# Kernel tuning notes

Measured on AMD Instinct MI355X. Metric: run time of the kernel, lower is better.

## Reference

```python
import jax, jax.numpy as jnp
import numpy as np

B, T, D = 4, 4096, 64

def setup_inputs() -> dict:
    key = jax.random.key(0)
    kq, kk, kv = jax.random.split(key, 3)
    Q = jax.random.normal(kq, (B, T, D), dtype=jnp.float32)
    K = jax.random.normal(kk, (B, T, D), dtype=jnp.float32)
    V = jax.random.normal(kv, (B, T, D), dtype=jnp.float32)
    mask = jnp.zeros((B, T, T), dtype=jnp.float32)
    return {"Q": Q, "K": K, "V": V, "mask": mask}

def reference(Q, K, V, mask):
    dk = Q.shape[-1]
    # NOTE: original scales by 1/dk (not 1/sqrt(dk)) -- reproduce faithfully.
    scores = jnp.einsum('btd,bsd->bts', Q, K) * (1.0 / dk)  # [B,T,T]
    scores = scores + mask
    attn = jax.nn.softmax(scores, axis=-1)
    return jnp.einsum('bts,bsd->btd', attn, V)  # [B,T,D]
```

## Files before the change

kernel.cpp:

```cpp
#include <hip/hip_runtime.h>
#include <stdint.h>

#define BB 4
#define TT 4096
#define DD 64
#define KBLK 64

typedef short short8 __attribute__((ext_vector_type(8)));
typedef float f32x4 __attribute__((ext_vector_type(4)));

__device__ __forceinline__ uint16_t f2bf(float x) {
  uint32_t u = __float_as_uint(x);
  u += 0x7FFFu + ((u >> 16) & 1u);
  return (uint16_t)(u >> 16);
}
__device__ __forceinline__ float bf2f(uint16_t h) {
  return __uint_as_float(((uint32_t)h) << 16);
}

#define MFMA(a, b, c) __builtin_amdgcn_mfma_f32_16x16x32_bf16((a), (b), (c), 0, 0, 0)

__global__ __launch_bounds__(256) void prep_kernel(
    const float* __restrict__ Q, const float* __restrict__ K, const float* __restrict__ V,
    uint16_t* __restrict__ Qh, uint16_t* __restrict__ Ql,
    uint16_t* __restrict__ Kh, uint16_t* __restrict__ Kl,
    uint16_t* __restrict__ Vh, uint16_t* __restrict__ Vl) {
  __shared__ float vt[64][65];
  const int blk = blockIdx.x;
  const int b = blk >> 6;
  const int r0 = (blk & 63) << 6;
  const int t = threadIdx.x;
  const size_t base = ((size_t)b * TT + r0) * DD;
  for (int i = t; i < 64 * 64; i += 256) {
    float q = Q[base + i] * 0.015625f;
    uint16_t h = f2bf(q);
    Qh[base + i] = h;
    Ql[base + i] = f2bf(q - bf2f(h));
    float k = K[base + i];
    h = f2bf(k);
    Kh[base + i] = h;
    Kl[base + i] = f2bf(k - bf2f(h));
    int r = i >> 6, c = i & 63;
    vt[r][c] = V[base + i];
  }
  __syncthreads();
  for (int i = t; i < 64 * 64; i += 256) {
    int d = i >> 6, c = i & 63;
    float v = vt[c][d];
    uint16_t h = f2bf(v);
    size_t o = ((size_t)b * DD + d) * TT + r0 + c;
    Vh[o] = h;
    Vl[o] = f2bf(v - bf2f(h));
  }
}

template <int NSEG, int NW>
__global__ __launch_bounds__(NW * 64, 4) void attn_kernel(
    const float* __restrict__ mask, float* __restrict__ out,
    float* __restrict__ Op, float* __restrict__ Mp, float* __restrict__ Lp,
    const uint16_t* __restrict__ Qh, const uint16_t* __restrict__ Ql,
    const uint16_t* __restrict__ Kh, const uint16_t* __restrict__ Kl,
    const uint16_t* __restrict__ Vh, const uint16_t* __restrict__ Vl) {
  constexpr int RPB = NW * 16;
  constexpr int PBH = (TT / RPB) / 2;
  constexpr int SEGLEN = TT / NSEG;
  constexpr int NIT = SEGLEN / KBLK;

  __shared__ uint16_t Kh_s[64][72], Kl_s[64][72];
  __shared__ uint16_t Vh_s[64][72], Vl_s[64][72];
  __shared__ uint16_t Ph_s[NW][16][72], Pl_s[NW][16][72];

  const int bid = blockIdx.x;
  const int xcd = bid & 7;
  const int b = xcd >> 1;
  const int u = bid >> 3;
  const int rbl = (u % PBH) * 2 + (xcd & 1);
  const int seg = u / PBH;
  const int q0 = rbl * RPB;
  const int t = threadIdx.x;
  const int w = t >> 6;
  const int l = t & 63;
  const int lr = l & 15;
  const int lq = l >> 4;
  const int qrow = q0 + w * 16;
  const int sb = seg * SEGLEN;

  const uint16_t* qhp = Qh + ((size_t)b * TT + qrow + lr) * DD + lq * 8;
  const uint16_t* qlp = Ql + ((size_t)b * TT + qrow + lr) * DD + lq * 8;
  short8 qh[2], ql[2];
  qh[0] = *(const short8*)(qhp);
  qh[1] = *(const short8*)(qhp + 32);
  ql[0] = *(const short8*)(qlp);
  ql[1] = *(const short8*)(qlp + 32);

  f32x4 o[4];
  float mrow[4], lrow[4];
#pragma unroll
  for (int dt = 0; dt < 4; ++dt) o[dt] = (f32x4){0.f, 0.f, 0.f, 0.f};
#pragma unroll
  for (int j = 0; j < 4; ++j) { mrow[j] = -1e30f; lrow[j] = 0.f; }

  const float* mp[4];
#pragma unroll
  for (int j = 0; j < 4; ++j)
    mp[j] = mask + ((size_t)b * TT + qrow + lq * 4 + j) * TT + sb + lr;

  float mk[16];
#pragma unroll
  for (int tt = 0; tt < 4; ++tt)
#pragma unroll
    for (int j = 0; j < 4; ++j)
      mk[tt * 4 + j] = __builtin_nontemporal_load(mp[j] + tt * 16);

  const size_t kvb = (size_t)b * TT * DD;
  const size_t vtb = (size_t)b * DD * TT;

  for (int it = 0; it < NIT; ++it) {
    const int s0 = sb + it * KBLK;
    __syncthreads();
    for (int i = t; i < 512; i += NW * 64) {
      const int row = i >> 3, c = i & 7;
      const size_t ko = kvb + (size_t)(s0 + row) * DD + c * 8;
      *(short8*)&Kh_s[row][c * 8] = *(const short8*)(Kh + ko);
      *(short8*)&Kl_s[row][c * 8] = *(const short8*)(Kl + ko);
      const size_t vo = vtb + (size_t)row * TT + s0 + c * 8;
      *(short8*)&Vh_s[row][c * 8] = *(const short8*)(Vh + vo);
      *(short8*)&Vl_s[row][c * 8] = *(const short8*)(Vl + vo);
    }
    __syncthreads();

    float mk2[16];
    if (it + 1 < NIT) {
#pragma unroll
      for (int tt = 0; tt < 4; ++tt)
#pragma unroll
        for (int j = 0; j < 4; ++j)
          mk2[tt * 4 + j] = __builtin_nontemporal_load(mp[j] + (it + 1) * KBLK + tt * 16);
    } else {
#pragma unroll
      for (int i = 0; i < 16; ++i) mk2[i] = 0.f;
    }

    f32x4 s[4];
#pragma unroll
    for (int tt = 0; tt < 4; ++tt) {
      f32x4 acc = (f32x4){0.f, 0.f, 0.f, 0.f};
#pragma unroll
      for (int c = 0; c < 2; ++c) {
        const short8 bh = *(const short8*)&Kh_s[tt * 16 + lr][c * 32 + lq * 8];
        const short8 bl = *(const short8*)&Kl_s[tt * 16 + lr][c * 32 + lq * 8];
        acc = MFMA(qh[c], bh, acc);
        acc = MFMA(ql[c], bh, acc);
        acc = MFMA(qh[c], bl, acc);
      }
      s[tt] = acc;
    }
#pragma unroll
    for (int tt = 0; tt < 4; ++tt)
#pragma unroll
      for (int j = 0; j < 4; ++j) s[tt][j] += mk[tt * 4 + j];

    float cm[4];
#pragma unroll
    for (int j = 0; j < 4; ++j)
      cm[j] = fmaxf(fmaxf(s[0][j], s[1][j]), fmaxf(s[2][j], s[3][j]));
#pragma unroll
    for (int d = 1; d < 16; d <<= 1)
#pragma unroll
      for (int j = 0; j < 4; ++j) cm[j] = fmaxf(cm[j], __shfl_xor(cm[j], d, 16));
    float scl[4];
#pragma unroll
    for (int j = 0; j < 4; ++j) {
      const float mn = fmaxf(mrow[j], cm[j]);
      scl[j] = __expf(mrow[j] - mn);
      mrow[j] = mn;
    }
#pragma unroll
    for (int tt = 0; tt < 4; ++tt)
#pragma unroll
      for (int j = 0; j < 4; ++j) s[tt][j] = __expf(s[tt][j] - mrow[j]);
    float rs[4];
#pragma unroll
    for (int j = 0; j < 4; ++j) rs[j] = (s[0][j] + s[1][j]) + (s[2][j] + s[3][j]);
#pragma unroll
    for (int d = 1; d < 16; d <<= 1)
#pragma unroll
      for (int j = 0; j < 4; ++j) rs[j] += __shfl_xor(rs[j], d, 16);
#pragma unroll
    for (int j = 0; j < 4; ++j) lrow[j] = lrow[j] * scl[j] + rs[j];
#pragma unroll
    for (int dt = 0; dt < 4; ++dt)
#pragma unroll
      for (int j = 0; j < 4; ++j) o[dt][j] *= scl[j];

#pragma unroll
    for (int tt = 0; tt < 4; ++tt)
#pragma unroll
      for (int j = 0; j < 4; ++j) {
        const float p = s[tt][j];
        const uint16_t h = f2bf(p);
        Ph_s[w][lq * 4 + j][tt * 16 + lr] = h;
        Pl_s[w][lq * 4 + j][tt * 16 + lr] = f2bf(p - bf2f(h));
      }

#pragma unroll
    for (int c = 0; c < 2; ++c) {
      const short8 ph = *(const short8*)&Ph_s[w][lr][c * 32 + lq * 8];
      const short8 pl = *(const short8*)&Pl_s[w][lr][c * 32 + lq * 8];
#pragma unroll
      for (int dt = 0; dt < 4; ++dt) {
        const short8 vh = *(const short8*)&Vh_s[dt * 16 + lr][c * 32 + lq * 8];
        const short8 vl = *(const short8*)&Vl_s[dt * 16 + lr][c * 32 + lq * 8];
        o[dt] = MFMA(ph, vh, o[dt]);
        o[dt] = MFMA(pl, vh, o[dt]);
        o[dt] = MFMA(ph, vl, o[dt]);
      }
    }

#pragma unroll
    for (int i = 0; i < 16; ++i) mk[i] = mk2[i];
  }

  if constexpr (NSEG == 1) {
#pragma unroll
    for (int j = 0; j < 4; ++j) {
      const float inv = 1.0f / lrow[j];
      const size_t ob = ((size_t)b * TT + qrow + lq * 4 + j) * DD + lr;
#pragma unroll
      for (int dt = 0; dt < 4; ++dt) out[ob + dt * 16] = o[dt][j] * inv;
    }
  } else {
    const int grow = b * TT + qrow + lq * 4;
#pragma unroll
    for (int j = 0; j < 4; ++j) {
      const size_t r = (size_t)seg * (BB * TT) + grow + j;
#pragma unroll
      for (int dt = 0; dt < 4; ++dt) Op[r * 64 + dt * 16 + lr] = o[dt][j];
      if (lr == 0) { Mp[r] = mrow[j]; Lp[r] = lrow[j]; }
    }
  }
}

__global__ __launch_bounds__(256) void combine_kernel(
    const float* __restrict__ Op, const float* __restrict__ Mp,
    const float* __restrict__ Lp, float* __restrict__ out, int nseg) {
  const int gid = blockIdx.x * 256 + threadIdx.x;
  const int r = gid >> 6, d = gid & 63;
  constexpr int ROWS = BB * TT;
  float m = -3.0e38f;
  for (int s = 0; s < nseg; ++s) m = fmaxf(m, Mp[s * ROWS + r]);
  float num = 0.f, den = 0.f;
  for (int s = 0; s < nseg; ++s) {
    const float e = __expf(Mp[s * ROWS + r] - m);
    den += Lp[s * ROWS + r] * e;
    num += Op[((size_t)s * ROWS + r) * 64 + d] * e;
  }
  out[(size_t)r * 64 + d] = num / den;
}

extern "C" void kernel_launch(void* const* d_in, const int* in_sizes, int n_in,
                              void* d_out, int out_size, void* d_ws, size_t ws_size,
                              hipStream_t stream) {
  const float* Q = (const float*)d_in[0];
  const float* K = (const float*)d_in[1];
  const float* V = (const float*)d_in[2];
  const float* mask = (const float*)d_in[3];
  float* out = (float*)d_out;

  const size_t NE = (size_t)BB * TT * DD;
  const size_t ROWS = (size_t)BB * TT;
  uint16_t* ws = (uint16_t*)d_ws;
  uint16_t* Qh = ws;
  uint16_t* Ql = ws + NE;
  uint16_t* Kh = ws + 2 * NE;
  uint16_t* Kl = ws + 3 * NE;
  uint16_t* Vh = ws + 4 * NE;
  uint16_t* Vl = ws + 5 * NE;

  const size_t bf_bytes = 6 * NE * 2;
  const size_t per_seg = ROWS * 64 * 4 + ROWS * 2 * 4;
  int nseg = (ws_size >= bf_bytes + 4 * per_seg) ? 4
           : (ws_size >= bf_bytes + 2 * per_seg) ? 2 : 1;

  char* pbase = (char*)d_ws + bf_bytes;
  float* Op = (float*)pbase;
  float* Mp = (float*)(pbase + (size_t)nseg * ROWS * 64 * 4);
  float* Lp = Mp + (size_t)nseg * ROWS;

  prep_kernel<<<dim3(256), dim3(256), 0, stream>>>(Q, K, V, Qh, Ql, Kh, Kl, Vh, Vl);

  if (nseg == 4) {
    attn_kernel<4, 8><<<dim3(512), dim3(512), 0, stream>>>(
        mask, out, Op, Mp, Lp, Qh, Ql, Kh, Kl, Vh, Vl);
  } else if (nseg == 2) {
    attn_kernel<2, 8><<<dim3(256), dim3(512), 0, stream>>>(
        mask, out, Op, Mp, Lp, Qh, Ql, Kh, Kl, Vh, Vl);
  } else {
    attn_kernel<1, 4><<<dim3(256), dim3(256), 0, stream>>>(
        mask, out, Op, Mp, Lp, Qh, Ql, Kh, Kl, Vh, Vl);
  }
  if (nseg > 1) {
    combine_kernel<<<dim3((ROWS * 64) / 256), dim3(256), 0, stream>>>(Op, Mp, Lp, out, nseg);
  }
}
```

Baseline: 422.5 us.

## Transpose QK MFMA so each lane owns a row, vectorize mask loads, lazy rescale

The QK^T MFMA operands are swapped so the score tile comes out transposed, with each lane holding four consecutive key columns of a single query row. The mask can then be read with 16-byte vector loads, row max and sum reductions need only two cross-lane shuffles instead of four per value, and P is written to LDS as packed 32-bit bf16 pairs. It also skips rescaling the output and running sum unless some row's max grows by more than 8, which cuts exp and multiply work. The cost is extra shuffles to redistribute per-row scales to the output layout, plus a wave-wide vote per iteration. Skipped rescales leave exponentials up to e^8, which is safe in fp32.

```diff
diff --git a/kernel.cpp b/kernel.cpp
--- a/kernel.cpp
+++ b/kernel.cpp
@@ -16,6 +16,9 @@
 }
 __device__ __forceinline__ float bf2f(uint16_t h) {
   return __uint_as_float(((uint32_t)h) << 16);
+}
+__device__ __forceinline__ uint32_t pkbf(float a, float b) {
+  return (uint32_t)f2bf(a) | ((uint32_t)f2bf(b) << 16);
 }
 
 #define MFMA(a, b, c) __builtin_amdgcn_mfma_f32_16x16x32_bf16((a), (b), (c), 0, 0, 0)
@@ -94,23 +97,16 @@
   ql[1] = *(const short8*)(qlp + 32);
 
   f32x4 o[4];
-  float mrow[4], lrow[4];
+  float mrow = -1e30f, lrow = 0.f;
 #pragma unroll
   for (int dt = 0; dt < 4; ++dt) o[dt] = (f32x4){0.f, 0.f, 0.f, 0.f};
-#pragma unroll
-  for (int j = 0; j < 4; ++j) { mrow[j] = -1e30f; lrow[j] = 0.f; }
-
-  const float* mp[4];
-#pragma unroll
-  for (int j = 0; j < 4; ++j)
-    mp[j] = mask + ((size_t)b * TT + qrow + lq * 4 + j) * TT + sb + lr;
-
-  float mk[16];
+
+  const float* mprow = mask + ((size_t)b * TT + qrow + lr) * TT + sb + lq * 4;
+
+  f32x4 mk[4];
 #pragma unroll
   for (int tt = 0; tt < 4; ++tt)
-#pragma unroll
-    for (int j = 0; j < 4; ++j)
-      mk[tt * 4 + j] = __builtin_nontemporal_load(mp[j] + tt * 16);
+    mk[tt] = __builtin_nontemporal_load((const f32x4*)(mprow + tt * 16));
 
   const size_t kvb = (size_t)b * TT * DD;
   const size_t vtb = (size_t)b * DD * TT;
@@ -129,16 +125,14 @@
     }
     __syncthreads();
 
-    float mk2[16];
+    f32x4 mk2[4];
     if (it + 1 < NIT) {
 #pragma unroll
       for (int tt = 0; tt < 4; ++tt)
-#pragma unroll
-        for (int j = 0; j < 4; ++j)
-          mk2[tt * 4 + j] = __builtin_nontemporal_load(mp[j] + (it + 1) * KBLK + tt * 16);
+        mk2[tt] = __builtin_nontemporal_load((const f32x4*)(mprow + (it + 1) * KBLK + tt * 16));
     } else {
 #pragma unroll
-      for (int i = 0; i < 16; ++i) mk2[i] = 0.f;
+      for (int tt = 0; tt < 4; ++tt) mk2[tt] = (f32x4){0.f, 0.f, 0.f, 0.f};
     }
 
     f32x4 s[4];
@@ -149,59 +143,56 @@
       for (int c = 0; c < 2; ++c) {
         const short8 bh = *(const short8*)&Kh_s[tt * 16 + lr][c * 32 + lq * 8];
         const short8 bl = *(const short8*)&Kl_s[tt * 16 + lr][c * 32 + lq * 8];
-        acc = MFMA(qh[c], bh, acc);
-        acc = MFMA(ql[c], bh, acc);
-        acc = MFMA(qh[c], bl, acc);
+        acc = MFMA(bh, qh[c], acc);
+        acc = MFMA(bl, qh[c], acc);
+        acc = MFMA(bh, ql[c], acc);
       }
       s[tt] = acc;
     }
 #pragma unroll
+    for (int tt = 0; tt < 4; ++tt) s[tt] += mk[tt];
+
+    float cm = fmaxf(fmaxf(fmaxf(s[0][0], s[0][1]), fmaxf(s[0][2], s[0][3])),
+                     fmaxf(fmaxf(s[1][0], s[1][1]), fmaxf(s[1][2], s[1][3])));
+    cm = fmaxf(cm, fmaxf(fmaxf(fmaxf(s[2][0], s[2][1]), fmaxf(s[2][2], s[2][3])),
+                         fmaxf(fmaxf(s[3][0], s[3][1]), fmaxf(s[3][2], s[3][3]))));
+    cm = fmaxf(cm, __shfl_xor(cm, 16));
+    cm = fmaxf(cm, __shfl_xor(cm, 32));
+    if (!__all(cm <= mrow + 8.0f)) {
+      const float mn = fmaxf(mrow, cm);
+      const float scl = __expf(mrow - mn);
+      mrow = mn;
+      lrow *= scl;
+      float sj[4];
+#pragma unroll
+      for (int j = 0; j < 4; ++j) sj[j] = __shfl(scl, lq * 4 + j);
+#pragma unroll
+      for (int dt = 0; dt < 4; ++dt)
+#pragma unroll
+        for (int j = 0; j < 4; ++j) o[dt][j] *= sj[j];
+    }
+#pragma unroll
     for (int tt = 0; tt < 4; ++tt)
 #pragma unroll
-      for (int j = 0; j < 4; ++j) s[tt][j] += mk[tt * 4 + j];
-
-    float cm[4];
-#pragma unroll
-    for (int j = 0; j < 4; ++j)
-      cm[j] = fmaxf(fmaxf(s[0][j], s[1][j]), fmaxf(s[2][j], s[3][j]));
-#pragma unroll
-    for (int d = 1; d < 16; d <<= 1)
-#pragma unroll
-      for (int j = 0; j < 4; ++j) cm[j] = fmaxf(cm[j], __shfl_xor(cm[j], d, 16));
-    float scl[4];
-#pragma unroll
-    for (int j = 0; j < 4; ++j) {
-      const float mn = fmaxf(mrow[j], cm[j]);
-      scl[j] = __expf(mrow[j] - mn);
-      mrow[j] = mn;
-    }
-#pragma unroll
-    for (int tt = 0; tt < 4; ++tt)
-#pragma unroll
-      for (int j = 0; j < 4; ++j) s[tt][j] = __expf(s[tt][j] - mrow[j]);
-    float rs[4];
-#pragma unroll
-    for (int j = 0; j < 4; ++j) rs[j] = (s[0][j] + s[1][j]) + (s[2][j] + s[3][j]);
-#pragma unroll
-    for (int d = 1; d < 16; d <<= 1)
-#pragma unroll
-      for (int j = 0; j < 4; ++j) rs[j] += __shfl_xor(rs[j], d, 16);
-#pragma unroll
-    for (int j = 0; j < 4; ++j) lrow[j] = lrow[j] * scl[j] + rs[j];
-#pragma unroll
-    for (int dt = 0; dt < 4; ++dt)
-#pragma unroll
-      for (int j = 0; j < 4; ++j) o[dt][j] *= scl[j];
-
-#pragma unroll
-    for (int tt = 0; tt < 4; ++tt)
-#pragma unroll
-      for (int j = 0; j < 4; ++j) {
-        const float p = s[tt][j];
-        const uint16_t h = f2bf(p);
-        Ph_s[w][lq * 4 + j][tt * 16 + lr] = h;
-        Pl_s[w][lq * 4 + j][tt * 16 + lr] = f2bf(p - bf2f(h));
-      }
+      for (int j = 0; j < 4; ++j) s[tt][j] = __expf(s[tt][j] - mrow);
+    float rs = ((s[0][0] + s[0][1]) + (s[0][2] + s[0][3])) +
+               ((s[1][0] + s[1][1]) + (s[1][2] + s[1][3])) +
+               ((s[2][0] + s[2][1]) + (s[2][2] + s[2][3])) +
+               ((s[3][0] + s[3][1]) + (s[3][2] + s[3][3]));
+    rs += __shfl_xor(rs, 16);
+    rs += __shfl_xor(rs, 32);
+    lrow += rs;
+
+#pragma unroll
+    for (int tt = 0; tt < 4; ++tt) {
+      float e0 = s[tt][0], e1 = s[tt][1], e2 = s[tt][2], e3 = s[tt][3];
+      *(uint32_t*)&Ph_s[w][lr][tt * 16 + lq * 4] = pkbf(e0, e1);
+      *(uint32_t*)&Ph_s[w][lr][tt * 16 + lq * 4 + 2] = pkbf(e2, e3);
+      float r0 = e0 - bf2f(f2bf(e0)), r1 = e1 - bf2f(f2bf(e1));
+      float r2 = e2 - bf2f(f2bf(e2)), r3 = e3 - bf2f(f2bf(e3));
+      *(uint32_t*)&Pl_s[w][lr][tt * 16 + lq * 4] = pkbf(r0, r1);
+      *(uint32_t*)&Pl_s[w][lr][tt * 16 + lq * 4 + 2] = pkbf(r2, r3);
+    }
 
 #pragma unroll
     for (int c = 0; c < 2; ++c) {
@@ -218,25 +209,30 @@
     }
 
 #pragma unroll
-    for (int i = 0; i < 16; ++i) mk[i] = mk2[i];
+    for (int tt = 0; tt < 4; ++tt) mk[tt] = mk2[tt];
   }
 
   if constexpr (NSEG == 1) {
+    const float linv = 1.0f / lrow;
 #pragma unroll
     for (int j = 0; j < 4; ++j) {
-      const float inv = 1.0f / lrow[j];
+      const float inv = __shfl(linv, lq * 4 + j);
       const size_t ob = ((size_t)b * TT + qrow + lq * 4 + j) * DD + lr;
 #pragma unroll
       for (int dt = 0; dt < 4; ++dt) out[ob + dt * 16] = o[dt][j] * inv;
     }
   } else {
-    const int grow = b * TT + qrow + lq * 4;
+    const int grow = b * TT + qrow;
 #pragma unroll
     for (int j = 0; j < 4; ++j) {
-      const size_t r = (size_t)seg * (BB * TT) + grow + j;
+      const size_t r = (size_t)seg * (BB * TT) + grow + lq * 4 + j;
 #pragma unroll
       for (int dt = 0; dt < 4; ++dt) Op[r * 64 + dt * 16 + lr] = o[dt][j];
-      if (lr == 0) { Mp[r] = mrow[j]; Lp[r] = lrow[j]; }
+    }
+    if (lq == 0) {
+      const size_t r = (size_t)seg * (BB * TT) + grow + lr;
+      Mp[r] = mrow;
+      Lp[r] = lrow;
     }
   }
 }
```

Measured after the change: 400.0 us. 1.06x faster.
